# Kernel tuning notes

Measured on AMD Instinct MI355X. Metric: run time of the kernel, lower is better.

Reference implementation:

```python
import jax, jax.numpy as jnp
import numpy as np

EMB_DIM = 512
QKV_DIM = 512
NUM_HEADS = 8
HEAD_DIM = QKV_DIM // NUM_HEADS
NUM_LANDMARKS = 64
N_ITER = 6


def setup_inputs() -> dict:
    key = jax.random.key(0)
    ks = jax.random.split(key, 9)
    s = 1.0 / np.sqrt(EMB_DIM)
    return {
        "x": jax.random.normal(ks[0], (4, 8192, EMB_DIM), dtype=jnp.float32),
        "Wq": jax.random.normal(ks[1], (EMB_DIM, QKV_DIM), dtype=jnp.float32) * s,
        "bq": jnp.zeros((QKV_DIM,), dtype=jnp.float32),
        "Wk": jax.random.normal(ks[2], (EMB_DIM, QKV_DIM), dtype=jnp.float32) * s,
        "bk": jnp.zeros((QKV_DIM,), dtype=jnp.float32),
        "Wv": jax.random.normal(ks[3], (EMB_DIM, QKV_DIM), dtype=jnp.float32) * s,
        "bv": jnp.zeros((QKV_DIM,), dtype=jnp.float32),
        "Wo": jax.random.normal(ks[4], (QKV_DIM, EMB_DIM), dtype=jnp.float32) * s,
        "bo": jnp.zeros((EMB_DIM,), dtype=jnp.float32),
    }


def _split_heads(x):
    bs, sl, _ = x.shape
    return x.reshape(bs, sl, NUM_HEADS, HEAD_DIM).transpose(0, 2, 1, 3)


def _iterative_inv(K):
    # K: [bs, h, L, L]; Newton-Schulz pseudo-inverse, 'original' init
    L = K.shape[-1]
    I = jnp.eye(L, dtype=K.dtype)
    V = K.swapaxes(-1, -2) / jnp.max(jnp.sum(K, axis=-2))
    for _ in range(N_ITER):
        KV = jnp.matmul(K, V)
        V = jnp.matmul(0.25 * V, 13.0 * I - jnp.matmul(KV, 15.0 * I - jnp.matmul(KV, 7.0 * I - KV)))
    return V


def reference(x, Wq, bq, Wk, bk, Wv, bv, Wo, bo):
    bs, seqlen, _ = x.shape
    # seqlen chosen divisible by NUM_LANDMARKS, so no padding branch
    full_len = seqlen
    q = _split_heads(x @ Wq + bq)
    k = _split_heads(x @ Wk + bk)
    v = _split_heads(x @ Wv + bv)
    scale = 1.0 / np.sqrt(np.sqrt(HEAD_DIM))
    q = q * scale
    k = k * scale

    seg = full_len // NUM_LANDMARKS
    q_land = q.reshape(bs, NUM_HEADS, NUM_LANDMARKS, seg, HEAD_DIM).mean(axis=-2)
    k_land = k.reshape(bs, NUM_HEADS, NUM_LANDMARKS, seg, HEAD_DIM).mean(axis=-2)

    kernel_1 = jax.nn.softmax(jnp.einsum('bhsd,bhld->bhsl', q, k_land), axis=-1)  # [bs,h,S,L]
    kernel_2 = jax.nn.softmax(jnp.einsum('bhld,bhmd->bhlm', q_land, k_land), axis=-1)  # [bs,h,L,L]
    kernel_3 = jax.nn.softmax(jnp.einsum('bhld,bhsd->bhls', q_land, k), axis=-1)  # [bs,h,L,S]

    out = jnp.matmul(jnp.matmul(kernel_1, _iterative_inv(kernel_2)), jnp.matmul(kernel_3, v))  # [bs,h,S,d]
    out = out.transpose(0, 2, 1, 3).reshape(bs, seqlen, QKV_DIM)
    return out @ Wo + bo
```

## Files before the change

kernel.cpp:

```cpp
#include <hip/hip_runtime.h>

#define BS 4
#define SEQL 8192
#define EMB 512
#define NH 8
#define HD 64
#define LM 64
#define SEG 128
#define BH (BS*NH)
#define NCH 16
#define CHS (SEQL/NCH)
#define QSCALE 0.35355339059327373f

typedef unsigned short u16;
typedef __bf16 bf16_t;
typedef __attribute__((ext_vector_type(8))) __bf16 bf16x8;
typedef __attribute__((ext_vector_type(4))) float f32x4;

#define MFMA16(a, b, c) __builtin_amdgcn_mfma_f32_16x16x32_bf16((a), (b), (c), 0, 0, 0)

__device__ __forceinline__ float bf2f(u16 u) {
  return __uint_as_float(((unsigned int)u) << 16);
}
__device__ __forceinline__ u16 f2bf(float f) {
  unsigned int u = __float_as_uint(f);
  u += 0x7fffu + ((u >> 16) & 1u);
  return (u16)(u >> 16);
}
__device__ __forceinline__ float load1_any(const void* p, size_t idx, int isf32) {
  return isf32 ? ((const float*)p)[idx] : bf2f(((const u16*)p)[idx]);
}
__device__ __forceinline__ void load4_any(const void* p, size_t idx, int isf32, float* dst) {
  if (isf32) {
    float4 v = *reinterpret_cast<const float4*>((const float*)p + idx);
    dst[0] = v.x; dst[1] = v.y; dst[2] = v.z; dst[3] = v.w;
  } else {
    ushort4 v = *reinterpret_cast<const ushort4*>((const u16*)p + idx);
    dst[0] = bf2f(v.x); dst[1] = bf2f(v.y); dst[2] = bf2f(v.z); dst[3] = bf2f(v.w);
  }
}
__device__ __forceinline__ void ld8_bf(const void* p, size_t idx, int isf32, u16* o) {
  if (isf32) {
    const float* f = (const float*)p + idx;
    float4 a = *reinterpret_cast<const float4*>(f);
    float4 b = *reinterpret_cast<const float4*>(f + 4);
    o[0] = f2bf(a.x); o[1] = f2bf(a.y); o[2] = f2bf(a.z); o[3] = f2bf(a.w);
    o[4] = f2bf(b.x); o[5] = f2bf(b.y); o[6] = f2bf(b.z); o[7] = f2bf(b.w);
  } else {
    *reinterpret_cast<int4*>(o) = *reinterpret_cast<const int4*>((const u16*)p + idx);
  }
}

__device__ __forceinline__ void async16(const void* g, void* l) {
  __builtin_amdgcn_global_load_lds(
      (const __attribute__((address_space(1))) void*)g,
      (__attribute__((address_space(3))) void*)l, 16, 0, 0);
}

__global__ __launch_bounds__(256) void probe_kernel(const void* x, int* flag) {
  __shared__ int cnt;
  if (threadIdx.x == 0) cnt = 0;
  __syncthreads();
  const u16* p = (const u16*)x;
  int c = 0;
  for (int j = 0; j < 16; j++) {
    u16 u = p[(size_t)(threadIdx.x * 16 + j) * 2];
    int e = (u >> 7) & 0xFF;
    if (e >= 134) c++;
  }
  atomicAdd(&cnt, c);
  __syncthreads();
  if (threadIdx.x == 0) flag[0] = (cnt > 256) ? 1 : 0;
}

__global__ __launch_bounds__(256) void prep_wt_kernel(
    const void* Wq, const void* Wk, const void* Wv, const void* Wo, const int* flag,
    u16* __restrict__ WqT, u16* __restrict__ WkT, u16* __restrict__ WvT, u16* __restrict__ WoT)
{
  __shared__ u16 Ws[64 * 72];
  const int id = blockIdx.x;
  const int z = id >> 6, tile = id & 63;
  const int k0 = (tile >> 3) * 64, n0 = (tile & 7) * 64;
  const void* W = (z == 0) ? Wq : (z == 1) ? Wk : (z == 2) ? Wv : Wo;
  u16* WT = (z == 0) ? WqT : (z == 1) ? WkT : (z == 2) ? WvT : WoT;
  const int isf32 = flag[0];
  const int t = threadIdx.x;
  const int r = t >> 2, cq = (t & 3) * 16;
  u16 tmp[8];
  #pragma unroll
  for (int u = 0; u < 2; u++) {
    ld8_bf(W, (size_t)(k0 + r) * EMB + n0 + cq + 8 * u, isf32, tmp);
    *reinterpret_cast<int4*>(&Ws[r * 72 + cq + 8 * u]) = *reinterpret_cast<int4*>(tmp);
  }
  __syncthreads();
  const int nn = t >> 2, kq = (t & 3) * 16;
  #pragma unroll
  for (int u = 0; u < 2; u++) {
    u16 o[8];
    #pragma unroll
    for (int j = 0; j < 8; j++) o[j] = Ws[(kq + 8 * u + j) * 72 + nn];
    *reinterpret_cast<int4*>(&WT[(size_t)(n0 + nn) * EMB + k0 + kq + 8 * u]) =
        *reinterpret_cast<int4*>(o);
  }
}

__global__ __launch_bounds__(256) void xpart_kernel(const void* x, const int* flag,
                                                    float* __restrict__ xpart,
                                                    u16* __restrict__ xb16) {
  __shared__ float red[512];
  const int blk = blockIdx.x;
  const int bl = blk >> 3, ch = blk & 7;
  const int t = threadIdx.x;
  const int isf32 = flag[0];
  const int rg = t >> 7;
  const int c4 = (t & 127) * 4;
  const size_t base = ((size_t)bl * SEG + ch * 16) * EMB;
  float s0 = 0.f, s1 = 0.f, s2 = 0.f, s3 = 0.f;
  for (int r = rg; r < 16; r += 2) {
    size_t idx = base + (size_t)r * EMB + c4;
    if (isf32) {
      float4 v = *reinterpret_cast<const float4*>((const float*)x + idx);
      ushort4 ob;
      ob.x = f2bf(v.x); ob.y = f2bf(v.y); ob.z = f2bf(v.z); ob.w = f2bf(v.w);
      *reinterpret_cast<ushort4*>(&xb16[idx]) = ob;
      s0 += v.x; s1 += v.y; s2 += v.z; s3 += v.w;
    } else {
      ushort4 v = *reinterpret_cast<const ushort4*>((const u16*)x + idx);
      s0 += bf2f(v.x); s1 += bf2f(v.y); s2 += bf2f(v.z); s3 += bf2f(v.w);
    }
  }
  if (rg == 0) {
    red[c4] = s0; red[c4 + 1] = s1; red[c4 + 2] = s2; red[c4 + 3] = s3;
  }
  __syncthreads();
  if (rg == 1) {
    red[c4] += s0; red[c4 + 1] += s1; red[c4 + 2] += s2; red[c4 + 3] += s3;
  }
  __syncthreads();
  if (t < 128) {
    float4 o;
    o.x = red[t * 4]; o.y = red[t * 4 + 1]; o.z = red[t * 4 + 2]; o.w = red[t * 4 + 3];
    *reinterpret_cast<float4*>(&xpart[(size_t)blk * 512 + t * 4]) = o;
  }
}

__global__ __launch_bounds__(256) void xmean_reduce_kernel(
    const float* __restrict__ xpart, float* __restrict__ xmean) {
  const int bl = blockIdx.x;
  const int t = threadIdx.x;
  const int c = t * 2;
  float s0 = 0.f, s1 = 0.f;
  #pragma unroll
  for (int ch = 0; ch < 8; ch++) {
    const float* p = &xpart[((size_t)(bl * 8 + ch)) * 512 + c];
    s0 += p[0]; s1 += p[1];
  }
  xmean[(size_t)bl * EMB + c]     = s0 * (1.0f / SEG);
  xmean[(size_t)bl * EMB + c + 1] = s1 * (1.0f / SEG);
}

__global__ __launch_bounds__(256) void lm_proj_kernel(
    const float* __restrict__ xmean,
    const void* Wq, const void* bq, const void* Wk, const void* bk,
    const int* flag, float* __restrict__ qL, float* __restrict__ kL,
    u16* __restrict__ qLb, u16* __restrict__ kLb)
{
  __shared__ float As[64 * 17];
  __shared__ float Bs[16 * 64];
  const int t = threadIdx.x;
  const int m0 = blockIdx.x * 64, n0 = blockIdx.y * 64, z = blockIdx.z;
  const void* W    = z ? Wk : Wq;
  const void* bias = z ? bk : bq;
  float* dst       = z ? kL : qL;
  u16*   dstb      = z ? kLb : qLb;
  const int isf32 = flag[0];
  const int tx = t & 15, ty = t >> 4;
  const int arow = t >> 2, akk = (t & 3) << 2;
  const int brow = t >> 4, bcol = (t & 15) << 2;
  float acc[4][4] = {};
  for (int k0 = 0; k0 < EMB; k0 += 16) {
    float4 av = *reinterpret_cast<const float4*>(xmean + (size_t)(m0 + arow) * EMB + k0 + akk);
    As[arow * 17 + akk + 0] = av.x;
    As[arow * 17 + akk + 1] = av.y;
    As[arow * 17 + akk + 2] = av.z;
    As[arow * 17 + akk + 3] = av.w;
    load4_any(W, (size_t)(k0 + brow) * EMB + n0 + bcol, isf32, &Bs[brow * 64 + bcol]);
    __syncthreads();
    #pragma unroll
    for (int kk = 0; kk < 16; kk++) {
      float a[4], b[4];
      #pragma unroll
      for (int i = 0; i < 4; i++) a[i] = As[(ty * 4 + i) * 17 + kk];
      #pragma unroll
      for (int j = 0; j < 4; j++) b[j] = Bs[kk * 64 + tx * 4 + j];
      #pragma unroll
      for (int i = 0; i < 4; i++)
        #pragma unroll
        for (int j = 0; j < 4; j++)
          acc[i][j] = fmaf(a[i], b[j], acc[i][j]);
    }
    __syncthreads();
  }
  #pragma unroll
  for (int i = 0; i < 4; i++) {
    int m = m0 + ty * 4 + i;
    int b = m >> 6, l = m & 63;
    #pragma unroll
    for (int j = 0; j < 4; j++) {
      int n = n0 + tx * 4 + j;
      int h = n >> 6, d = n & 63;
      float c = (acc[i][j] + load1_any(bias, n, isf32)) * QSCALE;
      size_t idx = (size_t)((b * NH + h) * LM + l) * HD + d;
      dst[idx] = c;
      dstb[idx] = f2bf(c);
    }
  }
}

__global__ __launch_bounds__(256, 2) void proj_qkv_fused_kernel(
    const void* x, const u16* __restrict__ xb16, const u16* __restrict__ WqT,
    const u16* __restrict__ WkT, const u16* __restrict__ WvT,
    const void* bq, const void* bk, const void* bv, const int* flag,
    u16* __restrict__ Qb, u16* __restrict__ Kb, u16* __restrict__ VbT)
{
  __shared__ u16 smem[2 * 128 * 64 + 2 * 3 * 64 * 64];
  u16* As = smem;
  u16* Bs = smem + 2 * 128 * 64;
  const int t = threadIdx.x;
  const int orig = blockIdx.x;
  const int swz  = (orig & 7) * 256 + (orig >> 3);
  const int h    = swz & 7;
  const int m0   = (swz >> 3) * 128;
  const int n0   = h * 64;
  const int isf32 = flag[0];
  const u16* xs = isf32 ? xb16 : (const u16*)x;
  const int w = t >> 6, lane = t & 63, q = lane >> 4, c = lane & 15;
  const int wm = (w >> 1) * 64, wn = (w & 1) * 32;
  const int row8 = lane >> 3;
  const int csw  = ((lane & 7) ^ row8) * 8;

  f32x4 acc[3][4][2];
  f32x4 z4 = {0.f, 0.f, 0.f, 0.f};
  #pragma unroll
  for (int z = 0; z < 3; z++)
    #pragma unroll
    for (int mi = 0; mi < 4; mi++) { acc[z][mi][0] = z4; acc[z][mi][1] = z4; }

  #pragma unroll
  for (int u = 0; u < 4; u++) {
    int ca = u * 4 + w;
    async16(&xs[(size_t)(m0 + ca * 8 + row8) * EMB + 0 + csw], &As[ca * 512]);
  }
  #pragma unroll
  for (int u = 0; u < 6; u++) {
    int cb = u * 4 + w, z = cb >> 3, r8 = cb & 7;
    const u16* Wt = (z == 0) ? WqT : (z == 1) ? WkT : WvT;
    async16(&Wt[(size_t)(n0 + r8 * 8 + row8) * EMB + 0 + csw],
            &Bs[z * 4096 + r8 * 512]);
  }
  __syncthreads();

  for (int tt = 0; tt < 8; tt++) {
    const int cur = tt & 1;
    if (tt < 7) {
      const int k1 = (tt + 1) * 64;
      const int nb = (cur ^ 1);
      #pragma unroll
      for (int u = 0; u < 4; u++) {
        int ca = u * 4 + w;
        async16(&xs[(size_t)(m0 + ca * 8 + row8) * EMB + k1 + csw],
                &As[nb * 8192 + ca * 512]);
      }
      #pragma unroll
      for (int u = 0; u < 6; u++) {
        int cb = u * 4 + w, z = cb >> 3, r8 = cb & 7;
        const u16* Wt = (z == 0) ? WqT : (z == 1) ? WkT : WvT;
        async16(&Wt[(size_t)(n0 + r8 * 8 + row8) * EMB + k1 + csw],
                &Bs[nb * 12288 + z * 4096 + r8 * 512]);
      }
    }
    #pragma unroll
    for (int kk = 0; kk < 64; kk += 32) {
      const int u0 = ((((kk >> 3) + q) ^ (c & 7))) * 8;
      bf16x8 af[4];
      #pragma unroll
      for (int mi = 0; mi < 4; mi++)
        af[mi] = *reinterpret_cast<const bf16x8*>(
            &As[cur * 8192 + (wm + mi * 16 + c) * 64 + u0]);
      #pragma unroll
      for (int z = 0; z < 3; z++) {
        bf16x8 b0v = *reinterpret_cast<const bf16x8*>(
            &Bs[cur * 12288 + z * 4096 + (wn + c) * 64 + u0]);
        bf16x8 b1v = *reinterpret_cast<const bf16x8*>(
            &Bs[cur * 12288 + z * 4096 + (wn + 16 + c) * 64 + u0]);
        #pragma unroll
        for (int mi = 0; mi < 4; mi++) {
          acc[z][mi][0] = MFMA16(af[mi], b0v, acc[z][mi][0]);
          acc[z][mi][1] = MFMA16(af[mi], b1v, acc[z][mi][1]);
        }
      }
    }
    __syncthreads();
  }

  float bb[3][2];
  #pragma unroll
  for (int z = 0; z < 3; z++) {
    const void* bias = (z == 0) ? bq : (z == 1) ? bk : bv;
    bb[z][0] = load1_any(bias, n0 + wn + c, isf32);
    bb[z][1] = load1_any(bias, n0 + wn + 16 + c, isf32);
  }
  const int b = m0 >> 13, s0t = m0 & (SEQL - 1);

  #pragma unroll
  for (int z = 0; z < 2; z++) {
    u16* dst = z ? Kb : Qb;
    #pragma unroll
    for (int mi = 0; mi < 4; mi++)
      #pragma unroll
      for (int i = 0; i < 4; i++) {
        int s = s0t + wm + mi * 16 + q * 4 + i;
        size_t rowb = ((size_t)((b * NH + h) * SEQL + s)) * HD;
        dst[rowb + wn + c]      = f2bf((acc[z][mi][0][i] + bb[z][0]) * QSCALE);
        dst[rowb + wn + 16 + c] = f2bf((acc[z][mi][1][i] + bb[z][1]) * QSCALE);
      }
  }

  __syncthreads();
  #pragma unroll
  for (int mi = 0; mi < 4; mi++)
    #pragma unroll
    for (int i = 0; i < 4; i++) {
      int ml = wm + mi * 16 + q * 4 + i;
      smem[(wn + c) * 136 + ml]      = f2bf(acc[2][mi][0][i] + bb[2][0]);
      smem[(wn + 16 + c) * 136 + ml] = f2bf(acc[2][mi][1][i] + bb[2][1]);
    }
  __syncthreads();
  const int nl = t >> 2, cq2 = (t & 3) * 32;
  #pragma unroll
  for (int u = 0; u < 4; u++)
    *reinterpret_cast<int4*>(&VbT[((size_t)((b * NH + h) * HD + nl)) * SEQL + s0t + cq2 + 8 * u]) =
        *reinterpret_cast<int4*>(&smem[nl * 136 + cq2 + 8 * u]);
}

__global__ __launch_bounds__(256) void k2_softmax_kernel(
    const float* __restrict__ qL, const float* __restrict__ kL,
    float* __restrict__ K2, float* __restrict__ cs)
{
  __shared__ float qs[64 * 65], ks[64 * 65], ps[64 * 65];
  const int t = threadIdx.x, bh = blockIdx.x;
  const int r = t >> 2, cb = (t & 3) << 4;
  #pragma unroll
  for (int i = 0; i < 16; i++) {
    qs[r * 65 + cb + i] = qL[((size_t)bh * LM + r) * HD + cb + i];
    ks[r * 65 + cb + i] = kL[((size_t)bh * LM + r) * HD + cb + i];
  }
  __syncthreads();
  float lg[16] = {};
  for (int d = 0; d < HD; d++) {
    float a = qs[r * 65 + d];
    #pragma unroll
    for (int i = 0; i < 16; i++) lg[i] = fmaf(a, ks[(cb + i) * 65 + d], lg[i]);
  }
  float m = lg[0];
  #pragma unroll
  for (int i = 1; i < 16; i++) m = fmaxf(m, lg[i]);
  m = fmaxf(m, __shfl_xor(m, 1));
  m = fmaxf(m, __shfl_xor(m, 2));
  float s = 0.f;
  #pragma unroll
  for (int i = 0; i < 16; i++) { lg[i] = __expf(lg[i] - m); s += lg[i]; }
  s += __shfl_xor(s, 1);
  s += __shfl_xor(s, 2);
  const float inv = 1.0f / s;
  #pragma unroll
  for (int i = 0; i < 16; i++) {
    float p = lg[i] * inv;
    ps[r * 65 + cb + i] = p;
    K2[((size_t)bh * LM + r) * LM + cb + i] = p;
  }
  __syncthreads();
  if (t < 64) {
    float c = 0.f;
    for (int rr = 0; rr < 64; rr++) c += ps[rr * 65 + t];
    cs[bh * LM + t] = c;
  }
}

__device__ __forceinline__ void mm_split(const u16* Ah, const u16* Al,
                                         const u16* Bh, const u16* Bl,
                                         int w, int lane, f32x4* out)
{
  const int q = lane >> 4, c = lane & 15;
  bf16x8 ah[2], al[2];
  #pragma unroll
  for (int k2 = 0; k2 < 2; k2++) {
    ah[k2] = *reinterpret_cast<const bf16x8*>(&Ah[(w * 16 + c) * 72 + k2 * 32 + q * 8]);
    al[k2] = *reinterpret_cast<const bf16x8*>(&Al[(w * 16 + c) * 72 + k2 * 32 + q * 8]);
  }
  #pragma unroll
  for (int nb = 0; nb < 4; nb++) {
    f32x4 acc = {0.f, 0.f, 0.f, 0.f};
    #pragma unroll
    for (int k2 = 0; k2 < 2; k2++) {
      bf16x8 bh_ = *reinterpret_cast<const bf16x8*>(&Bh[(nb * 16 + c) * 72 + k2 * 32 + q * 8]);
      bf16x8 bl_ = *reinterpret_cast<const bf16x8*>(&Bl[(nb * 16 + c) * 72 + k2 * 32 + q * 8]);
      acc = MFMA16(ah[k2], bh_, acc);
      acc = MFMA16(ah[k2], bl_, acc);
      acc = MFMA16(al[k2], bh_, acc);
    }
    out[nb] = acc;
  }
}

__global__ __launch_bounds__(256) void ns_inverse_kernel(
    const float* __restrict__ K2, const float* __restrict__ cs,
    float* __restrict__ Vi)
{
  __shared__ u16 K2h[64 * 72], K2l[64 * 72];
  __shared__ u16 VAh[64 * 72], VAl[64 * 72];
  __shared__ u16 VTh[64 * 72], VTl[64 * 72];
  __shared__ u16 KVh[64 * 72], KVl[64 * 72];
  __shared__ u16 Th [64 * 72], Tl [64 * 72];
  __shared__ float red[256];
  const int t = threadIdx.x, bh = blockIdx.x;
  const int w = t >> 6, lane = t & 63, q = lane >> 4, c = lane & 15;

  float m = -1e30f;
  for (int i = t; i < BH * LM; i += 256) m = fmaxf(m, cs[i]);
  red[t] = m;
  __syncthreads();
  for (int off = 128; off; off >>= 1) {
    if (t < off) red[t] = fmaxf(red[t], red[t + off]);
    __syncthreads();
  }
  const float ginv = 1.0f / red[0];
  __syncthreads();

  {
    const int r = t >> 2, cb = (t & 3) << 4;
    #pragma unroll
    for (int i = 0; i < 16; i++) {
      float v = K2[((size_t)bh * LM + r) * LM + cb + i];
      u16 h1 = f2bf(v);
      K2h[r * 72 + cb + i] = h1;
      K2l[r * 72 + cb + i] = f2bf(v - bf2f(h1));
      float sv = v * ginv;
      u16 h2 = f2bf(sv);
      u16 l2 = f2bf(sv - bf2f(h2));
      VTh[r * 72 + cb + i] = h2;
      VTl[r * 72 + cb + i] = l2;
      VAh[(cb + i) * 72 + r] = h2;
      VAl[(cb + i) * 72 + r] = l2;
    }
  }
  __syncthreads();

  f32x4 o[4];
  for (int it = 0; it < 6; it++) {
    mm_split(K2h, K2l, VTh, VTl, w, lane, o);
    __syncthreads();
    #pragma unroll
    for (int nb = 0; nb < 4; nb++)
      #pragma unroll
      for (int i = 0; i < 4; i++) {
        const int row = w * 16 + q * 4 + i, col = nb * 16 + c;
        const float v = o[nb][i];
        const u16 h1 = f2bf(v);
        KVh[row * 72 + col] = h1;
        KVl[row * 72 + col] = f2bf(v - bf2f(h1));
        const float tv = (row == col ? 7.0f : 0.0f) - v;
        const u16 h2 = f2bf(tv);
        Th[col * 72 + row] = h2;
        Tl[col * 72 + row] = f2bf(tv - bf2f(h2));
      }
    __syncthreads();
    mm_split(KVh, KVl, Th, Tl, w, lane, o);
    __syncthreads();
    #pragma unroll
    for (int nb = 0; nb < 4; nb++)
      #pragma unroll
      for (int i = 0; i < 4; i++) {
        const int row = w * 16 + q * 4 + i, col = nb * 16 + c;
        const float tv = (row == col ? 15.0f : 0.0f) - o[nb][i];
        const u16 h2 = f2bf(tv);
        Th[col * 72 + row] = h2;
        Tl[col * 72 + row] = f2bf(tv - bf2f(h2));
      }
    __syncthreads();
    mm_split(KVh, KVl, Th, Tl, w, lane, o);
    __syncthreads();
    #pragma unroll
    for (int nb = 0; nb < 4; nb++)
      #pragma unroll
      for (int i = 0; i < 4; i++) {
        const int row = w * 16 + q * 4 + i, col = nb * 16 + c;
        const float tv = (row == col ? 13.0f : 0.0f) - o[nb][i];
        const u16 h2 = f2bf(tv);
        Th[col * 72 + row] = h2;
        Tl[col * 72 + row] = f2bf(tv - bf2f(h2));
      }
    __syncthreads();
    mm_split(VAh, VAl, Th, Tl, w, lane, o);
    __syncthreads();
    #pragma unroll
    for (int nb = 0; nb < 4; nb++)
      #pragma unroll
      for (int i = 0; i < 4; i++) {
        const int row = w * 16 + q * 4 + i, col = nb * 16 + c;
        const float v = 0.25f * o[nb][i];
        const u16 h1 = f2bf(v);
        const u16 l1 = f2bf(v - bf2f(h1));
        VAh[row * 72 + col] = h1;
        VAl[row * 72 + col] = l1;
        VTh[col * 72 + row] = h1;
        VTl[col * 72 + row] = l1;
        if (it == 5) Vi[((size_t)bh * LM + row) * LM + col] = v;
      }
    __syncthreads();
  }
}

__global__ __launch_bounds__(256) void k3v_kernel(
    const u16* __restrict__ qLb, const u16* __restrict__ Kb, const u16* __restrict__ VbT,
    float* __restrict__ pnum, float* __restrict__ pden)
{
  __shared__ u16 Ks[64 * 72], Vs[2][64 * 72], Ps[64 * 72];
  __shared__ float denL[256];
  const int t = threadIdx.x, ch = blockIdx.x, bh = blockIdx.y;
  const int w = t >> 6, lane = t & 63, q = lane >> 4, c = lane & 15;
  const int sr = t >> 2, sp = (t & 3) * 16;

  bf16x8 aq[4][2];
  #pragma unroll
  for (int mi = 0; mi < 4; mi++)
    #pragma unroll
    for (int k2 = 0; k2 < 2; k2++)
      aq[mi][k2] = *reinterpret_cast<const bf16x8*>(
          &qLb[((size_t)bh * LM + mi * 16 + c) * HD + k2 * 32 + q * 8]);

  f32x4 z4 = {0.f, 0.f, 0.f, 0.f};
  f32x4 nacc[4];
  #pragma unroll
  for (int mi = 0; mi < 4; mi++) nacc[mi] = z4;
  float denr[16] = {};

  int4 kr0, kr1, vr0, vr1;
  {
    const int s0 = ch * CHS;
    const u16* kp = &Kb[((size_t)bh * SEQL + s0 + sr) * HD + sp];
    const u16* vp = &VbT[((size_t)(bh * HD + sr)) * SEQL + s0 + sp];
    kr0 = *reinterpret_cast<const int4*>(kp);
    kr1 = *reinterpret_cast<const int4*>(kp + 8);
    vr0 = *reinterpret_cast<const int4*>(vp);
    vr1 = *reinterpret_cast<const int4*>(vp + 8);
  }

  for (int sub = 0; sub < 8; sub++) {
    const int cur = sub & 1;
    *reinterpret_cast<int4*>(&Ks[sr * 72 + sp])     = kr0;
    *reinterpret_cast<int4*>(&Ks[sr * 72 + sp + 8]) = kr1;
    *reinterpret_cast<int4*>(&Vs[cur][sr * 72 + sp])     = vr0;
    *reinterpret_cast<int4*>(&Vs[cur][sr * 72 + sp + 8]) = vr1;
    __syncthreads();
    f32x4 sacc[4];
    #pragma unroll
    for (int mi = 0; mi < 4; mi++) sacc[mi] = z4;
    bf16x8 bk0 = *reinterpret_cast<const bf16x8*>(&Ks[(w * 16 + c) * 72 + q * 8]);
    bf16x8 bk1 = *reinterpret_cast<const bf16x8*>(&Ks[(w * 16 + c) * 72 + 32 + q * 8]);
    #pragma unroll
    for (int mi = 0; mi < 4; mi++) {
      sacc[mi] = MFMA16(aq[mi][0], bk0, sacc[mi]);
      sacc[mi] = MFMA16(aq[mi][1], bk1, sacc[mi]);
    }
    #pragma unroll
    for (int mi = 0; mi < 4; mi++)
      #pragma unroll
      for (int i = 0; i < 4; i++) {
        float p = __expf(sacc[mi][i]);
        denr[mi * 4 + i] += p;
        Ps[(mi * 16 + q * 4 + i) * 72 + w * 16 + c] = f2bf(p);
      }
    __syncthreads();
    if (sub < 7) {
      const int s1 = ch * CHS + (sub + 1) * 64;
      const u16* kp = &Kb[((size_t)bh * SEQL + s1 + sr) * HD + sp];
      const u16* vp = &VbT[((size_t)(bh * HD + sr)) * SEQL + s1 + sp];
      kr0 = *reinterpret_cast<const int4*>(kp);
      kr1 = *reinterpret_cast<const int4*>(kp + 8);
      vr0 = *reinterpret_cast<const int4*>(vp);
      vr1 = *reinterpret_cast<const int4*>(vp + 8);
    }
    #pragma unroll
    for (int k2 = 0; k2 < 2; k2++) {
      bf16x8 bv_ = *reinterpret_cast<const bf16x8*>(&Vs[cur][(w * 16 + c) * 72 + k2 * 32 + q * 8]);
      #pragma unroll
      for (int mi = 0; mi < 4; mi++) {
        bf16x8 ap = *reinterpret_cast<const bf16x8*>(&Ps[(mi * 16 + c) * 72 + k2 * 32 + q * 8]);
        nacc[mi] = MFMA16(ap, bv_, nacc[mi]);
      }
    }
  }
  #pragma unroll
  for (int mi = 0; mi < 4; mi++)
    #pragma unroll
    for (int i = 0; i < 4; i++)
      pnum[(((size_t)bh * NCH + ch) * LM + mi * 16 + q * 4 + i) * HD + w * 16 + c] = nacc[mi][i];
  #pragma unroll
  for (int v = 0; v < 16; v++) {
    denr[v] += __shfl_xor(denr[v], 1);
    denr[v] += __shfl_xor(denr[v], 2);
    denr[v] += __shfl_xor(denr[v], 4);
    denr[v] += __shfl_xor(denr[v], 8);
  }
  if (c == 0) {
    #pragma unroll
    for (int mi = 0; mi < 4; mi++)
      #pragma unroll
      for (int i = 0; i < 4; i++)
        denL[w * 64 + mi * 16 + q * 4 + i] = denr[mi * 4 + i];
  }
  __syncthreads();
  if (t < 64)
    pden[((size_t)bh * NCH + ch) * LM + t] = denL[t] + denL[64 + t] + denL[128 + t] + denL[192 + t];
}

__global__ __launch_bounds__(256) void k3v_w2_kernel(
    const float* __restrict__ pnum, const float* __restrict__ pden,
    const float* __restrict__ Vi, u16* __restrict__ W2T)
{
  __shared__ float Vs[64 * 65], Ms[64 * 65], den[64];
  const int t = threadIdx.x, bh = blockIdx.x;
  const int r = t >> 2, cb = (t & 3) << 4;
  #pragma unroll
  for (int i = 0; i < 16; i++) Vs[r * 65 + cb + i] = Vi[((size_t)bh * LM + r) * LM + cb + i];
  float acc[16] = {};
  for (int ch = 0; ch < NCH; ch++) {
    const float* p = pnum + (((size_t)bh * NCH + ch) * LM + r) * HD + cb;
    #pragma unroll
    for (int i = 0; i < 16; i++) acc[i] += p[i];
  }
  if ((t & 3) == 0) {
    float d = 0.f;
    for (int ch = 0; ch < NCH; ch++) d += pden[((size_t)bh * NCH + ch) * LM + r];
    den[r] = d;
  }
  __syncthreads();
  const float dinv = 1.0f / den[r];
  #pragma unroll
  for (int i = 0; i < 16; i++) Ms[r * 65 + cb + i] = acc[i] * dinv;
  __syncthreads();
  float o[16] = {};
  for (int k = 0; k < 64; k++) {
    float a = Vs[r * 65 + k];
    #pragma unroll
    for (int i = 0; i < 16; i++) o[i] = fmaf(a, Ms[k * 65 + cb + i], o[i]);
  }
  #pragma unroll
  for (int i = 0; i < 16; i++)
    W2T[((size_t)bh * HD + cb + i) * LM + r] = f2bf(o[i]);
}

__global__ __launch_bounds__(256) void final_kernel(
    const u16* __restrict__ Qb, const u16* __restrict__ kLb, const u16* __restrict__ W2T,
    u16* __restrict__ pre)
{
  __shared__ u16 Ps[64 * 72];
  __shared__ float mxL[256], smL[256];
  const int t = threadIdx.x, st = blockIdx.x, bh = blockIdx.y;
  const int w = t >> 6, lane = t & 63, q = lane >> 4, c = lane & 15;
  const int sb = st * 64;

  bf16x8 aq[4][2], bkL[2], bw2[2];
  #pragma unroll
  for (int mi = 0; mi < 4; mi++)
    #pragma unroll
    for (int k2 = 0; k2 < 2; k2++)
      aq[mi][k2] = *reinterpret_cast<const bf16x8*>(
          &Qb[((size_t)bh * SEQL + sb + mi * 16 + c) * HD + k2 * 32 + q * 8]);
  #pragma unroll
  for (int k2 = 0; k2 < 2; k2++) {
    bkL[k2] = *reinterpret_cast<const bf16x8*>(
        &kLb[((size_t)bh * LM + w * 16 + c) * HD + k2 * 32 + q * 8]);
    bw2[k2] = *reinterpret_cast<const bf16x8*>(
        &W2T[((size_t)bh * HD + w * 16 + c) * LM + k2 * 32 + q * 8]);
  }

  f32x4 z4 = {0.f, 0.f, 0.f, 0.f};
  f32x4 sacc[4];
  #pragma unroll
  for (int mi = 0; mi < 4; mi++) sacc[mi] = z4;
  #pragma unroll
  for (int k2 = 0; k2 < 2; k2++)
    #pragma unroll
    for (int mi = 0; mi < 4; mi++)
      sacc[mi] = MFMA16(aq[mi][k2], bkL[k2], sacc[mi]);

  float mx[16];
  #pragma unroll
  for (int v = 0; v < 16; v++) {
    mx[v] = sacc[v >> 2][v & 3];
    mx[v] = fmaxf(mx[v], __shfl_xor(mx[v], 1));
    mx[v] = fmaxf(mx[v], __shfl_xor(mx[v], 2));
    mx[v] = fmaxf(mx[v], __shfl_xor(mx[v], 4));
    mx[v] = fmaxf(mx[v], __shfl_xor(mx[v], 8));
  }
  if (c == 0) {
    #pragma unroll
    for (int mi = 0; mi < 4; mi++)
      #pragma unroll
      for (int i = 0; i < 4; i++)
        mxL[w * 64 + mi * 16 + q * 4 + i] = mx[mi * 4 + i];
  }
  __syncthreads();
  float p[16], dn[16];
  #pragma unroll
  for (int mi = 0; mi < 4; mi++)
    #pragma unroll
    for (int i = 0; i < 4; i++) {
      int row = mi * 16 + q * 4 + i;
      float M = fmaxf(fmaxf(mxL[row], mxL[64 + row]), fmaxf(mxL[128 + row], mxL[192 + row]));
      float pp = __expf(sacc[mi][i] - M);
      p[mi * 4 + i] = pp;
      dn[mi * 4 + i] = pp;
    }
  #pragma unroll
  for (int v = 0; v < 16; v++) {
    dn[v] += __shfl_xor(dn[v], 1);
    dn[v] += __shfl_xor(dn[v], 2);
    dn[v] += __shfl_xor(dn[v], 4);
    dn[v] += __shfl_xor(dn[v], 8);
  }
  if (c == 0) {
    #pragma unroll
    for (int mi = 0; mi < 4; mi++)
      #pragma unroll
      for (int i = 0; i < 4; i++)
        smL[w * 64 + mi * 16 + q * 4 + i] = dn[mi * 4 + i];
  }
  #pragma unroll
  for (int mi = 0; mi < 4; mi++)
    #pragma unroll
    for (int i = 0; i < 4; i++)
      Ps[(mi * 16 + q * 4 + i) * 72 + w * 16 + c] = f2bf(p[mi * 4 + i]);
  __syncthreads();

  f32x4 oacc[4];
  #pragma unroll
  for (int mi = 0; mi < 4; mi++) oacc[mi] = z4;
  #pragma unroll
  for (int k2 = 0; k2 < 2; k2++)
    #pragma unroll
    for (int mi = 0; mi < 4; mi++) {
      bf16x8 ap = *reinterpret_cast<const bf16x8*>(&Ps[(mi * 16 + c) * 72 + k2 * 32 + q * 8]);
      oacc[mi] = MFMA16(ap, bw2[k2], oacc[mi]);
    }
  #pragma unroll
  for (int mi = 0; mi < 4; mi++)
    #pragma unroll
    for (int i = 0; i < 4; i++) {
      int row = mi * 16 + q * 4 + i;
      float den = smL[row] + smL[64 + row] + smL[128 + row] + smL[192 + row];
      float v = oacc[mi][i] / den;
      pre[((size_t)((bh >> 3) * SEQL + sb + row)) * EMB + (bh & 7) * HD + w * 16 + c] = f2bf(v);
    }
}

__global__ __launch_bounds__(256, 2) void out_proj_kernel(
    const u16* __restrict__ pre, const u16* __restrict__ WoT, const void* bo,
    const int* flag, void* out)
{
  __shared__ u16 As[2 * 128 * 64];
  __shared__ u16 Bs[2 * 128 * 64];
  const int t = threadIdx.x;
  const int m0 = blockIdx.x * 128, n0 = blockIdx.y * 128;
  const int isf32 = flag[0];
  const int w = t >> 6, lane = t & 63, q = lane >> 4, c = lane & 15;
  const int wm = (w >> 1) * 64, wn = (w & 1) * 64;
  const int row8 = lane >> 3;
  const int colsw = ((lane & 7) ^ row8) * 8;

  f32x4 acc[4][4];
  f32x4 z4 = {0.f, 0.f, 0.f, 0.f};
  #pragma unroll
  for (int mi = 0; mi < 4; mi++)
    #pragma unroll
    for (int ni = 0; ni < 4; ni++) acc[mi][ni] = z4;

  #pragma unroll
  for (int u = 0; u < 4; u++) {
    int chA = u * 4 + w;
    async16(&pre[(size_t)(m0 + chA * 8 + row8) * EMB + 0 + colsw], &As[chA * 512]);
    async16(&WoT[(size_t)(n0 + chA * 8 + row8) * EMB + 0 + colsw], &Bs[chA * 512]);
  }
  __syncthreads();

  for (int tt = 0; tt < 8; tt++) {
    const int cur = tt & 1;
    if (tt < 7) {
      const int k1 = (tt + 1) * 64;
      #pragma unroll
      for (int u = 0; u < 4; u++) {
        int chA = u * 4 + w;
        async16(&pre[(size_t)(m0 + chA * 8 + row8) * EMB + k1 + colsw],
                &As[(cur ^ 1) * 8192 + chA * 512]);
        async16(&WoT[(size_t)(n0 + chA * 8 + row8) * EMB + k1 + colsw],
                &Bs[(cur ^ 1) * 8192 + chA * 512]);
      }
    }
    #pragma unroll
    for (int kk = 0; kk < 64; kk += 32) {
      const int u0 = ((((kk >> 3) + q) ^ (c & 7))) * 8;
      bf16x8 af[4], bfv[4];
      #pragma unroll
      for (int mi = 0; mi < 4; mi++)
        af[mi] = *reinterpret_cast<const bf16x8*>(&As[cur * 8192 + (wm + mi * 16 + c) * 64 + u0]);
      #pragma unroll
      for (int ni = 0; ni < 4; ni++)
        bfv[ni] = *reinterpret_cast<const bf16x8*>(&Bs[cur * 8192 + (wn + ni * 16 + c) * 64 + u0]);
      #pragma unroll
      for (int mi = 0; mi < 4; mi++)
        #pragma unroll
        for (int ni = 0; ni < 4; ni++)
          acc[mi][ni] = MFMA16(af[mi], bfv[ni], acc[mi][ni]);
    }
    __syncthreads();
  }
  float bb[4];
  #pragma unroll
  for (int ni = 0; ni < 4; ni++) bb[ni] = load1_any(bo, n0 + wn + ni * 16 + c, isf32);
  #pragma unroll
  for (int mi = 0; mi < 4; mi++)
    #pragma unroll
    for (int i = 0; i < 4; i++) {
      int m = m0 + wm + mi * 16 + q * 4 + i;
      #pragma unroll
      for (int ni = 0; ni < 4; ni++) {
        int n = n0 + wn + ni * 16 + c;
        float v = acc[mi][ni][i] + bb[ni];
        if (isf32) ((float*)out)[(size_t)m * EMB + n] = v;
        else       ((u16*)out)[(size_t)m * EMB + n] = f2bf(v);
      }
    }
}

extern "C" void kernel_launch(void* const* d_in, const int* in_sizes, int n_in,
                              void* d_out, int out_size, void* d_ws, size_t ws_size,
                              hipStream_t stream)
{
  (void)in_sizes; (void)n_in; (void)out_size; (void)ws_size;
  const void* x  = d_in[0];
  const void* Wq = d_in[1];
  const void* bq = d_in[2];
  const void* Wk = d_in[3];
  const void* bk = d_in[4];
  const void* Wv = d_in[5];
  const void* bv = d_in[6];
  const void* Wo = d_in[7];
  const void* bo = d_in[8];

  float* ws = (float*)d_ws;
  int*   flag  = (int*)ws;
  float* xmean = ws + 64;
  float* qL    = xmean + 131072;
  float* kL    = qL + 131072;
  float* K2    = kL + 131072;
  float* cs    = K2 + 131072;
  float* Vi    = cs + 2048;
  float* pnum  = Vi + 131072;
  float* pden  = pnum + 2097152;
  u16* WqT = (u16*)(pden + 32768);
  u16* WkT = WqT + 262144;
  u16* WvT = WkT + 262144;
  u16* WoT = WvT + 262144;
  u16* qLb = WoT + 262144;
  u16* kLb = qLb + 131072;
  u16* W2T = kLb + 131072;
  u16* Qb  = W2T + 131072;
  u16* Kb  = Qb + 16777216;
  u16* VbT = Kb + 16777216;
  u16* xb16 = VbT + 16777216;
  u16* pre = Kb;
  float* xpart = pnum;

  probe_kernel<<<1, 256, 0, stream>>>(x, flag);
  prep_wt_kernel<<<256, 256, 0, stream>>>(Wq, Wk, Wv, Wo, flag, WqT, WkT, WvT, WoT);
  xpart_kernel<<<2048, 256, 0, stream>>>(x, flag, xpart, xb16);
  xmean_reduce_kernel<<<256, 256, 0, stream>>>(xpart, xmean);
  lm_proj_kernel<<<dim3(4, 8, 2), 256, 0, stream>>>(xmean, Wq, bq, Wk, bk, flag, qL, kL, qLb, kLb);
  proj_qkv_fused_kernel<<<dim3(2048), 256, 0, stream>>>(
      x, xb16, WqT, WkT, WvT, bq, bk, bv, flag, Qb, Kb, VbT);
  k2_softmax_kernel<<<BH, 256, 0, stream>>>(qL, kL, K2, cs);
  ns_inverse_kernel<<<BH, 256, 0, stream>>>(K2, cs, Vi);
  k3v_kernel<<<dim3(NCH, BH), 256, 0, stream>>>(qLb, Kb, VbT, pnum, pden);
  k3v_w2_kernel<<<BH, 256, 0, stream>>>(pnum, pden, Vi, W2T);
  final_kernel<<<dim3(SEQL / 64, BH), 256, 0, stream>>>(Qb, kLb, W2T, pre);
  out_proj_kernel<<<dim3(256, 4), 256, 0, stream>>>(pre, WoT, bo, flag, d_out);
}
```

Measured before the change: 379.9 us.

## Fuse final attention stage with output projection, keeping pre-activation in LDS

Merges final_kernel and out_proj_kernel into one kernel. Each block handles 64 rows of one batch, loops over all 8 heads, and writes the bf16 attention output into an 80KB swizzled LDS tile instead of global memory. It then streams WoT tiles with double buffering to compute the output projection. This removes the global write and read of the pre tensor and one launch, at the cost of only 512 blocks, heavy LDS use that limits occupancy, and WoT being re-read by every block.

Measured after the change: 397.7 us. +4.7%, slower.

```diff
diff --git a/kernel.cpp b/kernel.cpp
--- a/kernel.cpp
+++ b/kernel.cpp
@@ -661,187 +661,183 @@
     W2T[((size_t)bh * HD + cb + i) * LM + r] = f2bf(o[i]);
 }
 
-__global__ __launch_bounds__(256) void final_kernel(
-    const u16* __restrict__ Qb, const u16* __restrict__ kLb, const u16* __restrict__ W2T,
-    u16* __restrict__ pre)
-{
-  __shared__ u16 Ps[64 * 72];
-  __shared__ float mxL[256], smL[256];
-  const int t = threadIdx.x, st = blockIdx.x, bh = blockIdx.y;
-  const int w = t >> 6, lane = t & 63, q = lane >> 4, c = lane & 15;
+__global__ __launch_bounds__(256, 2) void fused_out_kernel(
+    const u16* __restrict__ Qb, const u16* __restrict__ kLb,
+    const u16* __restrict__ W2T, const u16* __restrict__ WoT,
+    const void* bo, const int* flag, void* out)
+{
+  __shared__ u16 smem[40960];
+  u16* preS = smem;
+  u16* Ps   = smem + 32768;
+  float* mxL = (float*)(smem + 32768 + 4608);
+  float* smL = mxL + 256;
+  u16* Bs   = smem + 32768;
+  const int t = threadIdx.x;
+  const int b  = blockIdx.x >> 7;
+  const int st = blockIdx.x & 127;
   const int sb = st * 64;
-
-  bf16x8 aq[4][2], bkL[2], bw2[2];
-  #pragma unroll
-  for (int mi = 0; mi < 4; mi++)
-    #pragma unroll
-    for (int k2 = 0; k2 < 2; k2++)
-      aq[mi][k2] = *reinterpret_cast<const bf16x8*>(
-          &Qb[((size_t)bh * SEQL + sb + mi * 16 + c) * HD + k2 * 32 + q * 8]);
-  #pragma unroll
-  for (int k2 = 0; k2 < 2; k2++) {
-    bkL[k2] = *reinterpret_cast<const bf16x8*>(
-        &kLb[((size_t)bh * LM + w * 16 + c) * HD + k2 * 32 + q * 8]);
-    bw2[k2] = *reinterpret_cast<const bf16x8*>(
-        &W2T[((size_t)bh * HD + w * 16 + c) * LM + k2 * 32 + q * 8]);
-  }
-
-  f32x4 z4 = {0.f, 0.f, 0.f, 0.f};
-  f32x4 sacc[4];
-  #pragma unroll
-  for (int mi = 0; mi < 4; mi++) sacc[mi] = z4;
-  #pragma unroll
-  for (int k2 = 0; k2 < 2; k2++)
-    #pragma unroll
-    for (int mi = 0; mi < 4; mi++)
-      sacc[mi] = MFMA16(aq[mi][k2], bkL[k2], sacc[mi]);
-
-  float mx[16];
-  #pragma unroll
-  for (int v = 0; v < 16; v++) {
-    mx[v] = sacc[v >> 2][v & 3];
-    mx[v] = fmaxf(mx[v], __shfl_xor(mx[v], 1));
-    mx[v] = fmaxf(mx[v], __shfl_xor(mx[v], 2));
-    mx[v] = fmaxf(mx[v], __shfl_xor(mx[v], 4));
-    mx[v] = fmaxf(mx[v], __shfl_xor(mx[v], 8));
-  }
-  if (c == 0) {
-    #pragma unroll
-    for (int mi = 0; mi < 4; mi++)
-      #pragma unroll
-      for (int i = 0; i < 4; i++)
-        mxL[w * 64 + mi * 16 + q * 4 + i] = mx[mi * 4 + i];
-  }
-  __syncthreads();
-  float p[16], dn[16];
-  #pragma unroll
-  for (int mi = 0; mi < 4; mi++)
-    #pragma unroll
-    for (int i = 0; i < 4; i++) {
-      int row = mi * 16 + q * 4 + i;
-      float M = fmaxf(fmaxf(mxL[row], mxL[64 + row]), fmaxf(mxL[128 + row], mxL[192 + row]));
-      float pp = __expf(sacc[mi][i] - M);
-      p[mi * 4 + i] = pp;
-      dn[mi * 4 + i] = pp;
-    }
-  #pragma unroll
-  for (int v = 0; v < 16; v++) {
-    dn[v] += __shfl_xor(dn[v], 1);
-    dn[v] += __shfl_xor(dn[v], 2);
-    dn[v] += __shfl_xor(dn[v], 4);
-    dn[v] += __shfl_xor(dn[v], 8);
-  }
-  if (c == 0) {
-    #pragma unroll
-    for (int mi = 0; mi < 4; mi++)
-      #pragma unroll
-      for (int i = 0; i < 4; i++)
-        smL[w * 64 + mi * 16 + q * 4 + i] = dn[mi * 4 + i];
-  }
-  #pragma unroll
-  for (int mi = 0; mi < 4; mi++)
-    #pragma unroll
-    for (int i = 0; i < 4; i++)
-      Ps[(mi * 16 + q * 4 + i) * 72 + w * 16 + c] = f2bf(p[mi * 4 + i]);
-  __syncthreads();
-
-  f32x4 oacc[4];
-  #pragma unroll
-  for (int mi = 0; mi < 4; mi++) oacc[mi] = z4;
-  #pragma unroll
-  for (int k2 = 0; k2 < 2; k2++)
-    #pragma unroll
-    for (int mi = 0; mi < 4; mi++) {
-      bf16x8 ap = *reinterpret_cast<const bf16x8*>(&Ps[(mi * 16 + c) * 72 + k2 * 32 + q * 8]);
-      oacc[mi] = MFMA16(ap, bw2[k2], oacc[mi]);
-    }
-  #pragma unroll
-  for (int mi = 0; mi < 4; mi++)
-    #pragma unroll
-    for (int i = 0; i < 4; i++) {
-      int row = mi * 16 + q * 4 + i;
-      float den = smL[row] + smL[64 + row] + smL[128 + row] + smL[192 + row];
-      float v = oacc[mi][i] / den;
-      pre[((size_t)((bh >> 3) * SEQL + sb + row)) * EMB + (bh & 7) * HD + w * 16 + c] = f2bf(v);
-    }
-}
-
-__global__ __launch_bounds__(256, 2) void out_proj_kernel(
-    const u16* __restrict__ pre, const u16* __restrict__ WoT, const void* bo,
-    const int* flag, void* out)
-{
-  __shared__ u16 As[2 * 128 * 64];
-  __shared__ u16 Bs[2 * 128 * 64];
-  const int t = threadIdx.x;
-  const int m0 = blockIdx.x * 128, n0 = blockIdx.y * 128;
   const int isf32 = flag[0];
   const int w = t >> 6, lane = t & 63, q = lane >> 4, c = lane & 15;
-  const int wm = (w >> 1) * 64, wn = (w & 1) * 64;
   const int row8 = lane >> 3;
   const int colsw = ((lane & 7) ^ row8) * 8;
-
-  f32x4 acc[4][4];
   f32x4 z4 = {0.f, 0.f, 0.f, 0.f};
-  #pragma unroll
-  for (int mi = 0; mi < 4; mi++)
-    #pragma unroll
-    for (int ni = 0; ni < 4; ni++) acc[mi][ni] = z4;
-
-  #pragma unroll
-  for (int u = 0; u < 4; u++) {
-    int chA = u * 4 + w;
-    async16(&pre[(size_t)(m0 + chA * 8 + row8) * EMB + 0 + colsw], &As[chA * 512]);
-    async16(&WoT[(size_t)(n0 + chA * 8 + row8) * EMB + 0 + colsw], &Bs[chA * 512]);
-  }
-  __syncthreads();
-
-  for (int tt = 0; tt < 8; tt++) {
-    const int cur = tt & 1;
-    if (tt < 7) {
-      const int k1 = (tt + 1) * 64;
-      #pragma unroll
-      for (int u = 0; u < 4; u++) {
-        int chA = u * 4 + w;
-        async16(&pre[(size_t)(m0 + chA * 8 + row8) * EMB + k1 + colsw],
-                &As[(cur ^ 1) * 8192 + chA * 512]);
-        async16(&WoT[(size_t)(n0 + chA * 8 + row8) * EMB + k1 + colsw],
-                &Bs[(cur ^ 1) * 8192 + chA * 512]);
-      }
-    }
+
+  for (int h = 0; h < 8; h++) {
+    const int bh = b * 8 + h;
+    bf16x8 aq[4][2], bkL[2], bw2[2];
+    #pragma unroll
+    for (int mi = 0; mi < 4; mi++)
+      #pragma unroll
+      for (int k2 = 0; k2 < 2; k2++)
+        aq[mi][k2] = *reinterpret_cast<const bf16x8*>(
+            &Qb[((size_t)bh * SEQL + sb + mi * 16 + c) * HD + k2 * 32 + q * 8]);
+    #pragma unroll
+    for (int k2 = 0; k2 < 2; k2++) {
+      bkL[k2] = *reinterpret_cast<const bf16x8*>(
+          &kLb[((size_t)bh * LM + w * 16 + c) * HD + k2 * 32 + q * 8]);
+      bw2[k2] = *reinterpret_cast<const bf16x8*>(
+          &W2T[((size_t)bh * HD + w * 16 + c) * LM + k2 * 32 + q * 8]);
+    }
+
+    f32x4 sacc[4];
+    #pragma unroll
+    for (int mi = 0; mi < 4; mi++) sacc[mi] = z4;
+    #pragma unroll
+    for (int k2 = 0; k2 < 2; k2++)
+      #pragma unroll
+      for (int mi = 0; mi < 4; mi++)
+        sacc[mi] = MFMA16(aq[mi][k2], bkL[k2], sacc[mi]);
+
+    float mx[16];
+    #pragma unroll
+    for (int v = 0; v < 16; v++) {
+      mx[v] = sacc[v >> 2][v & 3];
+      mx[v] = fmaxf(mx[v], __shfl_xor(mx[v], 1));
+      mx[v] = fmaxf(mx[v], __shfl_xor(mx[v], 2));
+      mx[v] = fmaxf(mx[v], __shfl_xor(mx[v], 4));
+      mx[v] = fmaxf(mx[v], __shfl_xor(mx[v], 8));
+    }
+    if (c == 0) {
+      #pragma unroll
+      for (int mi = 0; mi < 4; mi++)
+        #pragma unroll
+        for (int i = 0; i < 4; i++)
+          mxL[w * 64 + mi * 16 + q * 4 + i] = mx[mi * 4 + i];
+    }
+    __syncthreads();
+    float p[16], dn[16];
+    #pragma unroll
+    for (int mi = 0; mi < 4; mi++)
+      #pragma unroll
+      for (int i = 0; i < 4; i++) {
+        int row = mi * 16 + q * 4 + i;
+        float M = fmaxf(fmaxf(mxL[row], mxL[64 + row]), fmaxf(mxL[128 + row], mxL[192 + row]));
+        float pp = __expf(sacc[mi][i] - M);
+        p[mi * 4 + i] = pp;
+        dn[mi * 4 + i] = pp;
+      }
+    #pragma unroll
+    for (int v = 0; v < 16; v++) {
+      dn[v] += __shfl_xor(dn[v], 1);
+      dn[v] += __shfl_xor(dn[v], 2);
+      dn[v] += __shfl_xor(dn[v], 4);
+      dn[v] += __shfl_xor(dn[v], 8);
+    }
+    if (c == 0) {
+      #pragma unroll
+      for (int mi = 0; mi < 4; mi++)
+        #pragma unroll
+        for (int i = 0; i < 4; i++)
+          smL[w * 64 + mi * 16 + q * 4 + i] = dn[mi * 4 + i];
+    }
+    #pragma unroll
+    for (int mi = 0; mi < 4; mi++)
+      #pragma unroll
+      for (int i = 0; i < 4; i++)
+        Ps[(mi * 16 + q * 4 + i) * 72 + w * 16 + c] = f2bf(p[mi * 4 + i]);
+    __syncthreads();
+
+    f32x4 oacc[4];
+    #pragma unroll
+    for (int mi = 0; mi < 4; mi++) oacc[mi] = z4;
+    #pragma unroll
+    for (int k2 = 0; k2 < 2; k2++)
+      #pragma unroll
+      for (int mi = 0; mi < 4; mi++) {
+        bf16x8 ap = *reinterpret_cast<const bf16x8*>(&Ps[(mi * 16 + c) * 72 + k2 * 32 + q * 8]);
+        oacc[mi] = MFMA16(ap, bw2[k2], oacc[mi]);
+      }
+    #pragma unroll
+    for (int mi = 0; mi < 4; mi++)
+      #pragma unroll
+      for (int i = 0; i < 4; i++) {
+        int row = mi * 16 + q * 4 + i;
+        float den = smL[row] + smL[64 + row] + smL[128 + row] + smL[192 + row];
+        float v = oacc[mi][i] / den;
+        int unit = (h << 3) + (w << 1) + (c >> 3);
+        int su = unit ^ (row & 7);
+        preS[row * 512 + su * 8 + (c & 7)] = f2bf(v);
+      }
+  }
+  __syncthreads();
+
+  #pragma unroll
+  for (int u = 0; u < 2; u++) {
+    int cb = u * 4 + w;
+    async16(&WoT[(size_t)(cb * 8 + row8) * EMB + 0 + colsw], &Bs[cb * 512]);
+  }
+  __syncthreads();
+
+  f32x4 acc[4];
+  #pragma unroll
+  for (int mi = 0; mi < 4; mi++) acc[mi] = z4;
+
+  for (int it = 0; it < 64; it++) {
+    const int cur = it & 1;
+    const int n0t = it >> 3, ks = it & 7;
+    if (it < 63) {
+      const int nn = it + 1;
+      const int n1 = (nn >> 3) * 64, k1 = (nn & 7) * 64;
+      #pragma unroll
+      for (int u = 0; u < 2; u++) {
+        int cb = u * 4 + w;
+        async16(&WoT[(size_t)(n1 + cb * 8 + row8) * EMB + k1 + colsw],
+                &Bs[(cur ^ 1) * 4096 + cb * 512]);
+      }
+    }
+    const int k0 = ks * 64;
     #pragma unroll
     for (int kk = 0; kk < 64; kk += 32) {
       const int u0 = ((((kk >> 3) + q) ^ (c & 7))) * 8;
-      bf16x8 af[4], bfv[4];
-      #pragma unroll
-      for (int mi = 0; mi < 4; mi++)
-        af[mi] = *reinterpret_cast<const bf16x8*>(&As[cur * 8192 + (wm + mi * 16 + c) * 64 + u0]);
-      #pragma unroll
-      for (int ni = 0; ni < 4; ni++)
-        bfv[ni] = *reinterpret_cast<const bf16x8*>(&Bs[cur * 8192 + (wn + ni * 16 + c) * 64 + u0]);
-      #pragma unroll
-      for (int mi = 0; mi < 4; mi++)
+      bf16x8 bfv = *reinterpret_cast<const bf16x8*>(
+          &Bs[cur * 4096 + (w * 16 + c) * 64 + u0]);
+      const int ku = ((k0 + kk) >> 3) + q;
+      const int su = (ku ^ (c & 7)) * 8;
+      #pragma unroll
+      for (int mi = 0; mi < 4; mi++) {
+        bf16x8 af = *reinterpret_cast<const bf16x8*>(&preS[(mi * 16 + c) * 512 + su]);
+        acc[mi] = MFMA16(af, bfv, acc[mi]);
+      }
+    }
+    if (ks == 7) {
+      const int n0 = n0t * 64;
+      const int ncol = n0 + w * 16 + c;
+      float bbv = load1_any(bo, ncol, isf32);
+      #pragma unroll
+      for (int mi = 0; mi < 4; mi++) {
         #pragma unroll
-        for (int ni = 0; ni < 4; ni++)
-          acc[mi][ni] = MFMA16(af[mi], bfv[ni], acc[mi][ni]);
-    }
-    __syncthreads();
-  }
-  float bb[4];
-  #pragma unroll
-  for (int ni = 0; ni < 4; ni++) bb[ni] = load1_any(bo, n0 + wn + ni * 16 + c, isf32);
-  #pragma unroll
-  for (int mi = 0; mi < 4; mi++)
-    #pragma unroll
-    for (int i = 0; i < 4; i++) {
-      int m = m0 + wm + mi * 16 + q * 4 + i;
-      #pragma unroll
-      for (int ni = 0; ni < 4; ni++) {
-        int n = n0 + wn + ni * 16 + c;
-        float v = acc[mi][ni][i] + bb[ni];
-        if (isf32) ((float*)out)[(size_t)m * EMB + n] = v;
-        else       ((u16*)out)[(size_t)m * EMB + n] = f2bf(v);
-      }
-    }
+        for (int i = 0; i < 4; i++) {
+          int row = mi * 16 + q * 4 + i;
+          float v = acc[mi][i] + bbv;
+          size_t oidx = ((size_t)(b * SEQL + sb + row)) * EMB + ncol;
+          if (isf32) ((float*)out)[oidx] = v;
+          else       ((u16*)out)[oidx] = f2bf(v);
+        }
+        acc[mi] = z4;
+      }
+    }
+    __syncthreads();
+  }
 }
 
 extern "C" void kernel_launch(void* const* d_in, const int* in_sizes, int n_in,
@@ -880,7 +876,6 @@
   u16* Kb  = Qb + 16777216;
   u16* VbT = Kb + 16777216;
   u16* xb16 = VbT + 16777216;
-  u16* pre = Kb;
   float* xpart = pnum;
 
   probe_kernel<<<1, 256, 0, stream>>>(x, flag);
@@ -894,6 +889,5 @@
   ns_inverse_kernel<<<BH, 256, 0, stream>>>(K2, cs, Vi);
   k3v_kernel<<<dim3(NCH, BH), 256, 0, stream>>>(qLb, Kb, VbT, pnum, pden);
   k3v_w2_kernel<<<BH, 256, 0, stream>>>(pnum, pden, Vi, W2T);
-  final_kernel<<<dim3(SEQL / 64, BH), 256, 0, stream>>>(Qb, kLb, W2T, pre);
-  out_proj_kernel<<<dim3(256, 4), 256, 0, stream>>>(pre, WoT, bo, flag, d_out);
-}
+  fused_out_kernel<<<dim3(512), 256, 0, stream>>>(Qb, kLb, W2T, WoT, bo, flag, d_out);
+}
```
